# Optimization experiments

Measured on AMD Instinct MI355X. Metric: run time of the kernel, lower is better.

Reference implementation:

```python
import jax, jax.numpy as jnp
import numpy as np

# static sizes (see shape_source)
OBJ_N, WALL_N, FLOOR_N = 192, 16, 1
T = OBJ_N + WALL_N + FLOOR_N          # 209 total nodes
R = T * T - T                          # 43472 directed edges (no self loops)
D = 512
STEPS = 4                              # feat_update_step (1 group)
OBJ_IN, WALL_IN, FLOOR_IN, REL_IN = 42, 15, 16, 2

# buildMap: all-pairs meshgrid edges, self-loops removed, one-hot subj/obj maps
_nd = ~np.eye(T, dtype=bool)
_si, _oi = np.meshgrid(np.arange(T), np.arange(T), indexing='ij')
_subj_idx = _si[_nd]
_obj_idx = _oi[_nd]
SUBJ_MAP = jnp.asarray((np.arange(T)[:, None] == _subj_idx[None, :]).astype(np.float32))  # [T,R]
OBJ_MAP = jnp.asarray((np.arange(T)[:, None] == _obj_idx[None, :]).astype(np.float32))    # [T,R]
TOTAL_MAP = jnp.ones((T, T), jnp.float32)
REL_IDX = jnp.asarray(np.nonzero(_nd.reshape(-1))[0])  # [R] static gather indices


def setup_inputs():
    key = jax.random.key(0)
    ks = iter(jax.random.split(key, 64))
    def w(shape):
        return jax.random.normal(next(ks), shape, jnp.float32) * 0.01  # normal_(0, 0.01)
    inp = {
        'cat_object_feature': jax.random.normal(next(ks), (1, OBJ_N, OBJ_IN), jnp.float32),
        'cat_wall_feature': jax.random.normal(next(ks), (1, WALL_N, WALL_IN), jnp.float32),
        'cat_floor_feature': jax.random.normal(next(ks), (1, FLOOR_N, FLOOR_IN), jnp.float32),
        'cat_relation_feature': jax.random.normal(next(ks), (1, OBJ_N * OBJ_N, REL_IN), jnp.float32),
    }
    for name, din in [('obj', OBJ_IN), ('wall', WALL_IN), ('floor', FLOOR_IN), ('rel', REL_IN)]:
        inp[name + '_w1'] = w((din, D)); inp[name + '_b1'] = jnp.zeros((D,), jnp.float32)
        inp[name + '_w2'] = w((D, D));   inp[name + '_b2'] = jnp.zeros((D,), jnp.float32)
    inp['collect_w'] = w((5, D, D))                       # 5 _Collection_Unit fc weights
    inp['collect_b'] = jnp.zeros((5, D), jnp.float32)
    for name in ['tr', 'eu', 'sc']:
        inp[name + '_w1'] = w((D, D // 2)); inp[name + '_b1'] = jnp.zeros((D // 2,), jnp.float32)
        inp[name + '_w2'] = w((D // 2, 3)); inp[name + '_b2'] = jnp.zeros((3,), jnp.float32)
    return inp


def _mlp(x, w1, b1, w2, b2):
    return jax.nn.relu(x @ w1 + b1) @ w2 + b2


def _head(x, w1, b1, w2, b2):
    # Linear -> LeakyReLU(0.2) -> Dropout(eval: identity) -> Linear
    return jax.nn.leaky_relu(x @ w1 + b1, 0.2) @ w2 + b2


def _collect(src, attn, w, b):
    # _Collection_Unit: attn @ relu(fc(src)) / (row_sum + 1e-7)
    fc = jax.nn.relu(src @ w + b)
    return (attn @ fc) / (attn.sum(1, keepdims=True) + 1e-7)


def reference(cat_object_feature, cat_wall_feature, cat_floor_feature, cat_relation_feature,
              obj_w1, obj_b1, obj_w2, obj_b2, wall_w1, wall_b1, wall_w2, wall_b2,
              floor_w1, floor_b1, floor_w2, floor_b2, rel_w1, rel_b1, rel_w2, rel_b2,
              collect_w, collect_b, tr_w1, tr_b1, tr_w2, tr_b2,
              eu_w1, eu_b1, eu_w2, eu_b2, sc_w1, sc_b1, sc_w2, sc_b2):
    tot = jnp.concatenate([
        _mlp(cat_object_feature[0], obj_w1, obj_b1, obj_w2, obj_b2),
        _mlp(cat_wall_feature[0], wall_w1, wall_b1, wall_w2, wall_b2),
        _mlp(cat_floor_feature[0], floor_w1, floor_b1, floor_w2, floor_b2)], axis=0)  # [T,D]
    emb_rel = _mlp(cat_relation_feature[0], rel_w1, rel_b1, rel_w2, rel_b2)
    padded = jnp.pad(emb_rel.reshape(OBJ_N, OBJ_N, D),
                     ((0, T - OBJ_N), (0, T - OBJ_N), (0, 0)), constant_values=0.001)
    rel = padded.reshape(T * T, D)[REL_IDX]  # mask_total_relation_feature [R,D]

    for _ in range(STEPS):
        s_obj = _collect(tot, TOTAL_MAP, collect_w[4], collect_b[4])
        s_rs = _collect(rel, SUBJ_MAP, collect_w[0], collect_b[0])
        s_ro = _collect(rel, OBJ_MAP, collect_w[1], collect_b[1])
        new_tot = tot + (s_obj + s_rs + s_ro) / 3.0          # _Update_Unit: target + source
        s_os = _collect(tot, SUBJ_MAP.T, collect_w[2], collect_b[2])
        s_oo = _collect(tot, OBJ_MAP.T, collect_w[3], collect_b[3])
        rel = rel + (s_os + s_oo) / 2.0
        tot = new_tot

    obj = tot[:OBJ_N]  # object_mask select
    return jnp.concatenate([
        _head(obj, tr_w1, tr_b1, tr_w2, tr_b2),
        _head(obj, eu_w1, eu_b1, eu_w2, eu_b2),
        _head(obj, sc_w1, sc_b1, sc_w2, sc_b2)], axis=-1)  # [OBJ_N, 9]
```

## Files before the change

kernel.cpp:

```cpp
#include <hip/hip_runtime.h>
#include <stdint.h>

typedef unsigned short u16;
typedef __attribute__((ext_vector_type(4))) float f32x4;
typedef __attribute__((ext_vector_type(8))) short s16x8;
typedef __attribute__((ext_vector_type(4))) short s16x4;

#define DD (512*512)

__device__ inline u16 f2bf(float f) {
  uint32_t u = __float_as_uint(f);
  u = (u + 0x7FFFu + ((u >> 16) & 1u)) >> 16;
  return (u16)u;
}
__device__ inline float bflo(uint32_t w) { return __uint_as_float(w << 16); }
__device__ inline float bfhi(uint32_t w) { return __uint_as_float(w & 0xFFFF0000u); }
__device__ inline f32x4 relu4(f32x4 v) {
  f32x4 r;
  r.x = fmaxf(v.x, 0.f); r.y = fmaxf(v.y, 0.f);
  r.z = fmaxf(v.z, 0.f); r.w = fmaxf(v.w, 0.f);
  return r;
}
__device__ inline f32x4 bf4(const u16* p) {
  uint2 w = *(const uint2*)p;
  f32x4 r; r.x = bflo(w.x); r.y = bfhi(w.x); r.z = bflo(w.y); r.w = bfhi(w.y);
  return r;
}
__device__ inline s16x4 pack4(f32x4 v) {
  s16x4 o;
  o[0] = (short)f2bf(v.x); o[1] = (short)f2bf(v.y);
  o[2] = (short)f2bf(v.z); o[3] = (short)f2bf(v.w);
  return o;
}
__device__ inline void gload16(const void* g, void* l) {
  __builtin_amdgcn_global_load_lds(
      (const __attribute__((address_space(1))) void*)g,
      (__attribute__((address_space(3))) void*)l, 16, 0, 0);
}

__global__ __launch_bounds__(256) void ktotl1(const float* __restrict__ xo, const float* __restrict__ xw,
                                              const float* __restrict__ xf,
                                              const float* __restrict__ ow1, const float* __restrict__ ob1,
                                              const float* __restrict__ ww1, const float* __restrict__ wb1,
                                              const float* __restrict__ fw1, const float* __restrict__ fb1,
                                              float* __restrict__ hid) {
  int tc = blockIdx.x;
  const float* x; const float* w; const float* b; int K;
  if (tc < 192)      { x = xo + tc * 42;        w = ow1; b = ob1; K = 42; }
  else if (tc < 208) { x = xw + (tc - 192) * 15; w = ww1; b = wb1; K = 15; }
  else               { x = xf;                   w = fw1; b = fb1; K = 16; }
  __shared__ float xs[48];
  int t = threadIdx.x;
  if (t < K) xs[t] = x[t];
  __syncthreads();
  #pragma unroll
  for (int dd = 0; dd < 2; dd++) {
    int d = t + dd * 256;
    float acc = b[d];
    for (int k = 0; k < K; k++) acc = fmaf(xs[k], w[k * 512 + d], acc);
    hid[(size_t)tc * 512 + d] = fmaxf(acc, 0.f);
  }
}

struct SJob { const float* A; const float* B; const float* bias; float* C; u16* Cb; int M; int act; };
struct SJobs { SJob j[8]; int cum[9]; int njobs; };

__global__ __launch_bounds__(256) void ksmall(SJobs js) {
  int bi = blockIdx.x;
  int ji = 0;
  while (ji + 1 < js.njobs && bi >= js.cum[ji + 1]) ji++;
  SJob job = js.j[ji];
  int local = bi - js.cum[ji];
  int mt = local >> 3, nt = local & 7;
  int m0 = mt * 32, n0 = nt * 64;

  __shared__ float As[32 * 36];
  __shared__ float Bs[32 * 64];
  int t = threadIdx.x;
  int row = t >> 3;
  int cg  = (t & 7) * 8;
  f32x4 accA = {0.f,0.f,0.f,0.f}, accB = {0.f,0.f,0.f,0.f};

  for (int k0 = 0; k0 < 512; k0 += 32) {
    __syncthreads();
    {
      int ar = t >> 3, ac = (t & 7) * 4;
      f32x4 av = {0.f,0.f,0.f,0.f};
      if (m0 + ar < job.M) av = *(const f32x4*)&job.A[(size_t)(m0 + ar) * 512 + k0 + ac];
      *(f32x4*)&As[ar * 36 + ac] = av;
    }
    #pragma unroll
    for (int i = 0; i < 2; i++) {
      int idx = t + i * 256;
      int bk = idx >> 4, bn = (idx & 15) * 4;
      *(f32x4*)&Bs[bk * 64 + bn] = *(const f32x4*)&job.B[(size_t)(k0 + bk) * 512 + n0 + bn];
    }
    __syncthreads();
    #pragma unroll
    for (int kk = 0; kk < 32; kk += 4) {
      f32x4 a4 = *(const f32x4*)&As[row * 36 + kk];
      #pragma unroll
      for (int q = 0; q < 4; q++) {
        f32x4 b0 = *(const f32x4*)&Bs[(kk + q) * 64 + cg];
        f32x4 b1 = *(const f32x4*)&Bs[(kk + q) * 64 + cg + 4];
        float av = a4[q];
        accA += av * b0;
        accB += av * b1;
      }
    }
  }
  int r = m0 + row;
  if (r < job.M) {
    f32x4 b0 = {0.f,0.f,0.f,0.f}, b1 = {0.f,0.f,0.f,0.f};
    if (job.bias) { b0 = *(const f32x4*)&job.bias[n0 + cg]; b1 = *(const f32x4*)&job.bias[n0 + cg + 4]; }
    f32x4 o0 = accA + b0, o1 = accB + b1;
    if (job.act) { o0 = relu4(o0); o1 = relu4(o1); }
    *(f32x4*)&job.C[(size_t)r * 512 + n0 + cg]     = o0;
    *(f32x4*)&job.C[(size_t)r * 512 + n0 + cg + 4] = o1;
    if (job.Cb) {
      s16x8 ob;
      ob[0] = (short)f2bf(o0.x); ob[1] = (short)f2bf(o0.y);
      ob[2] = (short)f2bf(o0.z); ob[3] = (short)f2bf(o0.w);
      ob[4] = (short)f2bf(o1.x); ob[5] = (short)f2bf(o1.y);
      ob[6] = (short)f2bf(o1.z); ob[7] = (short)f2bf(o1.w);
      *(s16x8*)&job.Cb[(size_t)r * 512 + n0 + cg] = ob;
    }
  }
}

__global__ __launch_bounds__(256) void kcast(const float* __restrict__ src, u16* __restrict__ dst) {
  int g = blockIdx.x * 256 + threadIdx.x;
  f32x4 a = *(const f32x4*)&src[(size_t)g * 8];
  f32x4 b = *(const f32x4*)&src[(size_t)g * 8 + 4];
  s16x8 o;
  o[0] = (short)f2bf(a.x); o[1] = (short)f2bf(a.y); o[2] = (short)f2bf(a.z); o[3] = (short)f2bf(a.w);
  o[4] = (short)f2bf(b.x); o[5] = (short)f2bf(b.y); o[6] = (short)f2bf(b.z); o[7] = (short)f2bf(b.w);
  *(s16x8*)&dst[(size_t)g * 8] = o;
}

__global__ __launch_bounds__(256) void kwcast(const float* __restrict__ cw, u16* __restrict__ cwT) {
  __shared__ float tile[32][33];
  const float* src = cw + (size_t)blockIdx.z * DD;
  int k0 = blockIdx.x * 32, n0 = blockIdx.y * 32;
  int t = threadIdx.x;
  #pragma unroll
  for (int i = 0; i < 4; i++) {
    int idx = t + i * 256; int r = idx >> 5, c = idx & 31;
    tile[r][c] = src[(size_t)(k0 + r) * 512 + n0 + c];
  }
  __syncthreads();
  #pragma unroll
  for (int i = 0; i < 4; i++) {
    int idx = t + i * 256; int r = idx >> 5, c = idx & 31;
    cwT[((size_t)blockIdx.z * 512 + n0 + r) * 512 + k0 + c] = f2bf(tile[c][r]);
  }
}

__global__ __launch_bounds__(256) void kwct(const float* __restrict__ tmp0, const float* __restrict__ tmp1,
                                            u16* __restrict__ WcT) {
  __shared__ float tile[32][33];
  const float* src = blockIdx.z ? tmp1 : tmp0;
  int k0 = blockIdx.x * 32, n0 = blockIdx.y * 32;
  int t = threadIdx.x;
  #pragma unroll
  for (int i = 0; i < 4; i++) {
    int idx = t + i * 256; int r = idx >> 5, c = idx & 31;
    tile[r][c] = src[(size_t)(k0 + r) * 512 + n0 + c];
  }
  __syncthreads();
  #pragma unroll
  for (int i = 0; i < 4; i++) {
    int idx = t + i * 256; int r = idx >> 5, c = idx & 31;
    WcT[((size_t)blockIdx.z * 512 + n0 + r) * 512 + k0 + c] = f2bf(tile[c][r]);
  }
}

__global__ __launch_bounds__(256) void kmisc(const float* __restrict__ cw, const float* __restrict__ cb,
                                             const float* __restrict__ rb2,
                                             float* __restrict__ b0b, float* __restrict__ b0p,
                                             float* __restrict__ b1b, float* __restrict__ b1p) {
  int t = threadIdx.x;
  int dl = t & 63;
  int d = blockIdx.x * 64 + dl;
  int kg = t >> 6;
  const float* W0 = cw;
  const float* W1 = cw + DD;
  float a0 = 0, p0 = 0, a1 = 0, p1 = 0;
  for (int k = kg * 128; k < (kg + 1) * 128; ++k) {
    float w0 = W0[(size_t)k * 512 + d], w1 = W1[(size_t)k * 512 + d], r = rb2[k];
    a0 = fmaf(r, w0, a0); p0 += w0;
    a1 = fmaf(r, w1, a1); p1 += w1;
  }
  __shared__ float red[4][4][64];
  red[0][kg][dl] = a0; red[1][kg][dl] = p0; red[2][kg][dl] = a1; red[3][kg][dl] = p1;
  __syncthreads();
  if (kg == 0) {
    float s0  = red[0][0][dl] + red[0][1][dl] + red[0][2][dl] + red[0][3][dl];
    float sp0 = red[1][0][dl] + red[1][1][dl] + red[1][2][dl] + red[1][3][dl];
    float s1  = red[2][0][dl] + red[2][1][dl] + red[2][2][dl] + red[2][3][dl];
    float sp1 = red[3][0][dl] + red[3][1][dl] + red[3][2][dl] + red[3][3][dl];
    float bb0 = cb[0 * 512 + d], bb1 = cb[1 * 512 + d];
    b0b[d] = s0 + bb0;
    b0p[d] = 0.001f * sp0 + bb0;
    b1b[d] = s1 + bb1;
    b1p[d] = 0.001f * sp1 + bb1;
  }
}

__global__ __launch_bounds__(256) void kH(const float* __restrict__ xr, const float* __restrict__ rw1,
                                          const float* __restrict__ rb1, u16* __restrict__ Hh) {
  int gid = blockIdx.x * 256 + threadIdx.x;
  int m = gid >> 6;
  int dg = (gid & 63) * 8;
  float x0 = xr[m * 2], x1 = xr[m * 2 + 1];
  s16x8 o;
  #pragma unroll
  for (int j = 0; j < 8; j++) {
    int dd = dg + j;
    float v = fmaf(x0, rw1[dd], fmaf(x1, rw1[512 + dd], rb1[dd]));
    o[j] = (short)f2bf(fmaxf(v, 0.f));
  }
  *(s16x8*)&Hh[(size_t)m * 512 + dg] = o;
}

struct MJob { const u16* A; const u16* BT; const float* bias; float* C; int Mreal; int act; };
struct MJobs { MJob j[8]; int cum[9]; int njobs; };

__global__ __launch_bounds__(256) void kmg(MJobs js) {
  int bi = blockIdx.x;
  int ji = 0;
  while (ji + 1 < js.njobs && bi >= js.cum[ji + 1]) ji++;
  MJob job = js.j[ji];
  int local = bi - js.cum[ji];
  int m0 = (local >> 2) * 64, n0 = (local & 3) * 128;

  __shared__ u16 smem[2 * 12288];
  const int t = threadIdx.x;
  const int lane = t & 63;
  const int wave = t >> 6;
  const int wm = wave >> 1, wn = wave & 1;
  const int r16 = lane & 15;
  const int kq = lane >> 4;
  f32x4 acc[2][4];
  #pragma unroll
  for (int i = 0; i < 2; i++)
    #pragma unroll
    for (int j = 0; j < 4; j++) acc[i][j] = (f32x4){0.f,0.f,0.f,0.f};

  const u16* gA[2]; int laofs[2];
  const u16* gB[4]; int lbofs[4];
  #pragma unroll
  for (int i = 0; i < 2; i++) {
    int seg = i * 256 + t;
    int row = seg >> 3, s = seg & 7;
    gA[i] = job.A + (size_t)(m0 + row) * 512 + ((s ^ (row & 7)) << 3);
    laofs[i] = (i * 256 + (t & 192)) << 3;
  }
  #pragma unroll
  for (int i = 0; i < 4; i++) {
    int seg = i * 256 + t;
    int row = seg >> 3, s = seg & 7;
    gB[i] = job.BT + (size_t)(n0 + row) * 512 + ((s ^ (row & 7)) << 3);
    lbofs[i] = 4096 + ((i * 256 + (t & 192)) << 3);
  }

  #pragma unroll
  for (int i = 0; i < 2; i++) gload16(gA[i], smem + laofs[i]);
  #pragma unroll
  for (int i = 0; i < 4; i++) gload16(gB[i], smem + lbofs[i]);
  __syncthreads();

  int buf = 0;
  for (int it = 0; it < 8; ++it) {
    if (it < 7) {
      int nb = (buf ^ 1) * 12288;
      int k0n = (it + 1) * 64;
      #pragma unroll
      for (int i = 0; i < 2; i++) gload16(gA[i] + k0n, smem + nb + laofs[i]);
      #pragma unroll
      for (int i = 0; i < 4; i++) gload16(gB[i] + k0n, smem + nb + lbofs[i]);
    }
    const u16* Ab = smem + buf * 12288;
    const u16* Bb = Ab + 4096;
    #pragma unroll
    for (int kh = 0; kh < 2; kh++) {
      s16x8 af[2], bfr[4];
      #pragma unroll
      for (int i = 0; i < 2; i++) {
        int r = wm * 32 + i * 16 + r16;
        af[i] = *(const s16x8*)&Ab[r * 64 + (((kq + kh * 4) ^ (r & 7)) << 3)];
      }
      #pragma unroll
      for (int j = 0; j < 4; j++) {
        int r = wn * 64 + j * 16 + r16;
        bfr[j] = *(const s16x8*)&Bb[r * 64 + (((kq + kh * 4) ^ (r & 7)) << 3)];
      }
      #pragma unroll
      for (int i = 0; i < 2; i++)
        #pragma unroll
        for (int j = 0; j < 4; j++)
          acc[i][j] = __builtin_amdgcn_mfma_f32_16x16x32_bf16(af[i], bfr[j], acc[i][j], 0, 0, 0);
    }
    __syncthreads();
    buf ^= 1;
  }

  float bj[4] = {0.f, 0.f, 0.f, 0.f};
  if (job.bias) {
    #pragma unroll
    for (int j = 0; j < 4; j++) bj[j] = job.bias[n0 + wn * 64 + j * 16 + r16];
  }
  #pragma unroll
  for (int i = 0; i < 2; i++) {
    int rbase = m0 + wm * 32 + i * 16 + (lane >> 4) * 4;
    #pragma unroll
    for (int r = 0; r < 4; r++) {
      int grow = rbase + r;
      if (grow < job.Mreal) {
        #pragma unroll
        for (int j = 0; j < 4; j++) {
          float v = acc[i][j][r] + bj[j];
          if (job.act) v = fmaxf(v, 0.f);
          job.C[(size_t)grow * 512 + n0 + wn * 64 + j * 16 + r16] = v;
        }
      }
    }
  }
}

__global__ __launch_bounds__(256) void kbig(const u16* __restrict__ Hh, const u16* __restrict__ WcT,
                                            u16* __restrict__ Q0, u16* __restrict__ Q1T) {
  __shared__ u16 smem[2 * 16384];
  const int m0 = blockIdx.y * 128;
  const int n0 = blockIdx.x * 128;
  const int t = threadIdx.x;
  const int lane = t & 63;
  const int wave = t >> 6;
  const int wm = wave >> 1, wn = wave & 1;
  const int r16 = lane & 15;
  const int kq = lane >> 4;
  f32x4 acc[4][4];
  #pragma unroll
  for (int i = 0; i < 4; i++)
    #pragma unroll
    for (int j = 0; j < 4; j++) acc[i][j] = (f32x4){0.f, 0.f, 0.f, 0.f};

  const u16* gA[4]; const u16* gB[4];
  int lofs[4];
  #pragma unroll
  for (int i = 0; i < 4; i++) {
    int seg = i * 256 + t;
    int row = seg >> 3, s = seg & 7;
    int sw = (s ^ (row & 7)) << 3;
    gA[i] = Hh  + (size_t)(m0 + row) * 512 + sw;
    gB[i] = WcT + (size_t)(n0 + row) * 512 + sw;
    lofs[i] = (i * 256 + (t & 192)) << 3;
  }

  #pragma unroll
  for (int i = 0; i < 4; i++) {
    gload16(gA[i], smem + lofs[i]);
    gload16(gB[i], smem + 8192 + lofs[i]);
  }
  __syncthreads();

  int buf = 0;
  for (int it = 0; it < 8; ++it) {
    if (it < 7) {
      int nb = (buf ^ 1) * 16384;
      int k0n = (it + 1) * 64;
      #pragma unroll
      for (int i = 0; i < 4; i++) {
        gload16(gA[i] + k0n, smem + nb + lofs[i]);
        gload16(gB[i] + k0n, smem + nb + 8192 + lofs[i]);
      }
    }
    const u16* Ab = smem + buf * 16384;
    const u16* Bb = Ab + 8192;
    #pragma unroll
    for (int kh = 0; kh < 2; kh++) {
      s16x8 af[4], bfr[4];
      #pragma unroll
      for (int i = 0; i < 4; i++) {
        int r = wm * 64 + i * 16 + r16;
        af[i] = *(const s16x8*)&Ab[r * 64 + (((kq + kh * 4) ^ (r & 7)) << 3)];
      }
      #pragma unroll
      for (int j = 0; j < 4; j++) {
        int r = wn * 64 + j * 16 + r16;
        bfr[j] = *(const s16x8*)&Bb[r * 64 + (((kq + kh * 4) ^ (r & 7)) << 3)];
      }
      #pragma unroll
      for (int i = 0; i < 4; i++)
        #pragma unroll
        for (int j = 0; j < 4; j++)
          acc[i][j] = __builtin_amdgcn_mfma_f32_16x16x32_bf16(af[i], bfr[j], acc[i][j], 0, 0, 0);
    }
    __syncthreads();
    buf ^= 1;
  }

  float* Cs = (float*)smem;
  const bool isQ1 = (n0 >= 512);
  #pragma unroll
  for (int c = 0; c < 4; c++) {
    __syncthreads();
    if ((c >> 1) == wm) {
      const int cbase = (c & 1) * 32;
      #pragma unroll
      for (int ii = 0; ii < 2; ii++) {
        const int i = (cbase >> 4) + ii;
        #pragma unroll
        for (int j = 0; j < 4; j++) {
          #pragma unroll
          for (int r = 0; r < 4; r++) {
            int rrow = i * 16 + (lane >> 4) * 4 + r - cbase;
            int ccol = wn * 64 + j * 16 + r16;
            Cs[rrow * 132 + ccol] = acc[i][j][r];
          }
        }
      }
    }
    __syncthreads();
    const int row = t >> 3, cg = (t & 7) * 16;
    const int gm = m0 + c * 32 + row;
    s16x8 o0, o1;
    #pragma unroll
    for (int x = 0; x < 8; x++) o0[x] = (short)f2bf(Cs[row * 132 + cg + x]);
    #pragma unroll
    for (int x = 0; x < 8; x++) o1[x] = (short)f2bf(Cs[row * 132 + cg + 8 + x]);
    u16* dst;
    if (!isQ1) {
      dst = Q0 + (size_t)gm * 512 + (n0 + cg);
    } else {
      int s = gm / 192, o = gm - s * 192;
      dst = Q1T + ((size_t)o * 192 + s) * 512 + (n0 - 512 + cg);
    }
    *(s16x8*)dst = o0;
    *(s16x8*)(dst + 8) = o1;
  }
}

__global__ __launch_bounds__(128) void kpass(const u16* __restrict__ Q0, const u16* __restrict__ Q1T,
                                             const float* __restrict__ u0, const float* __restrict__ v0,
                                             const float* __restrict__ u1, const float* __restrict__ v1,
                                             const float* __restrict__ b0b, const float* __restrict__ b1b,
                                             const float* __restrict__ fc4,
                                             float* __restrict__ part, float* __restrict__ sobj) {
  int z = blockIdx.z;
  int t = threadIdx.x;
  if (z == 2) {
    if (blockIdx.y != 0 || blockIdx.x >= 4) return;
    int d = blockIdx.x * 128 + t;
    float s = 0.f;
    for (int r = 0; r < 209; ++r) s += fc4[(size_t)r * 512 + d];
    sobj[d] = s;
    return;
  }
  int so = blockIdx.x;
  if (so >= 192) return;
  int chunk = blockIdx.y;
  int d = t * 4;
  const u16* Q = z ? Q1T : Q0;
  const float* fixtab  = z ? v1 : u0;
  const float* looptab = z ? u1 : v0;
  const float* bb = z ? b1b : b0b;
  f32x4 fix = *(const f32x4*)&fixtab[(size_t)so * 512 + d] + *(const f32x4*)&bb[d];
  f32x4 acc = {0.f,0.f,0.f,0.f};
  const u16* qbase = Q + ((size_t)so * 192 + chunk * 48) * 512 + d;
  const float* lbase = looptab + (size_t)(chunk * 48) * 512 + d;
  #pragma unroll 4
  for (int r = 0; r < 48; ++r) {
    f32x4 qa = bf4(qbase + (size_t)r * 512);
    f32x4 vv = *(const f32x4*)(lbase + (size_t)r * 512);
    f32x4 val = qa + fix + vv;
    acc.x += fmaxf(val.x, 0.f); acc.y += fmaxf(val.y, 0.f);
    acc.z += fmaxf(val.z, 0.f); acc.w += fmaxf(val.w, 0.f);
  }
  *(f32x4*)&part[(((size_t)z * 209 + so) * 4 + chunk) * 512 + d] = acc;
}

__global__ __launch_bounds__(128) void kfinish(const u16* __restrict__ Q0, const u16* __restrict__ Q1T,
                                               const float* __restrict__ u0, const float* __restrict__ v0,
                                               const float* __restrict__ u1, const float* __restrict__ v1,
                                               const float* __restrict__ b0b, const float* __restrict__ b0p,
                                               const float* __restrict__ b1b, const float* __restrict__ b1p,
                                               const float* __restrict__ part, const float* __restrict__ sobj,
                                               const float* __restrict__ fcS, const float* __restrict__ fcO,
                                               float* __restrict__ tot, float* __restrict__ addS,
                                               float* __restrict__ addO,
                                               u16* __restrict__ totb, u16* __restrict__ aSb,
                                               u16* __restrict__ aOb) {
  int tt = blockIdx.x;
  int t = threadIdx.x;
  int d = t * 4;
  size_t rowoff = (size_t)tt * 512 + d;
  f32x4 u0r = *(const f32x4*)&u0[rowoff];
  f32x4 v0r = *(const f32x4*)&v0[rowoff];
  f32x4 u1r = *(const f32x4*)&u1[rowoff];
  f32x4 v1r = *(const f32x4*)&v1[rowoff];
  f32x4 B0B = *(const f32x4*)&b0b[d];
  f32x4 B0P = *(const f32x4*)&b0p[d];
  f32x4 B1B = *(const f32x4*)&b1b[d];
  f32x4 B1P = *(const f32x4*)&b1p[d];
  f32x4 srs = {0.f,0.f,0.f,0.f}, sro = {0.f,0.f,0.f,0.f};
  if (tt < 192) {
    #pragma unroll
    for (int c = 0; c < 4; c++) {
      srs += *(const f32x4*)&part[(((size_t)0 * 209 + tt) * 4 + c) * 512 + d];
      sro += *(const f32x4*)&part[(((size_t)1 * 209 + tt) * 4 + c) * 512 + d];
    }
    for (int o = 192; o < 209; o++) srs += relu4(B0P + u0r + *(const f32x4*)&v0[(size_t)o * 512 + d]);
    for (int s = 192; s < 209; s++) sro += relu4(B1P + *(const f32x4*)&u1[(size_t)s * 512 + d] + v1r);
    f32x4 qd0 = bf4(Q0 + ((size_t)tt * 193) * 512 + d);
    srs -= relu4(qd0 + u0r + v0r + B0B);
    f32x4 qd1 = bf4(Q1T + ((size_t)tt * 193) * 512 + d);
    sro -= relu4(qd1 + u1r + v1r + B1B);
  } else {
    for (int o = 0; o < 209; o++) srs += relu4(B0P + u0r + *(const f32x4*)&v0[(size_t)o * 512 + d]);
    srs -= relu4(B0P + u0r + v0r);
    for (int s = 0; s < 209; s++) sro += relu4(B1P + *(const f32x4*)&u1[(size_t)s * 512 + d] + v1r);
    sro -= relu4(B1P + u1r + v1r);
// ... 57 lines not shown
    }
    __syncthreads();
  }
  if (t < 9) {
    const float* B2[3] = {b2a, b2b, b2c};
    out[(size_t)row * 9 + t] = red[t][0] + B2[t / 3][t % 3];
  }
}

extern "C" void kernel_launch(void* const* d_in, const int* in_sizes, int n_in,
                              void* d_out, int out_size, void* d_ws, size_t ws_size,
                              hipStream_t stream) {
  const float* xo  = (const float*)d_in[0];
  const float* xw  = (const float*)d_in[1];
  const float* xf  = (const float*)d_in[2];
  const float* xr  = (const float*)d_in[3];
  const float* ow1 = (const float*)d_in[4];
  const float* ob1 = (const float*)d_in[5];
  const float* ow2 = (const float*)d_in[6];
  const float* ob2 = (const float*)d_in[7];
  const float* ww1 = (const float*)d_in[8];
  const float* wb1 = (const float*)d_in[9];
  const float* ww2 = (const float*)d_in[10];
  const float* wb2 = (const float*)d_in[11];
  const float* fw1 = (const float*)d_in[12];
  const float* fb1 = (const float*)d_in[13];
  const float* fw2 = (const float*)d_in[14];
  const float* fb2 = (const float*)d_in[15];
  const float* rw1 = (const float*)d_in[16];
  const float* rb1 = (const float*)d_in[17];
  const float* rw2 = (const float*)d_in[18];
  const float* rb2 = (const float*)d_in[19];
  const float* cw  = (const float*)d_in[20];
  const float* cb  = (const float*)d_in[21];
  const float* tw1 = (const float*)d_in[22];
  const float* tb1 = (const float*)d_in[23];
  const float* tw2 = (const float*)d_in[24];
  const float* tb2 = (const float*)d_in[25];
  const float* ew1 = (const float*)d_in[26];
  const float* eb1 = (const float*)d_in[27];
  const float* ew2 = (const float*)d_in[28];
  const float* eb2 = (const float*)d_in[29];
  const float* sw1 = (const float*)d_in[30];
  const float* sb1 = (const float*)d_in[31];
  const float* sw2 = (const float*)d_in[32];
  const float* sb2 = (const float*)d_in[33];
  float* out = (float*)d_out;

  char* p = (char*)d_ws;
  auto alloc = [&](size_t bytes) { char* r = p; p += (bytes + 255) & ~(size_t)255; return r; };
  const size_t SZ = 209 * 512 * sizeof(float);
  const size_t BSZ = 256 * 512 * sizeof(u16);
  float* tot  = (float*)alloc(SZ);
  float* addS = (float*)alloc(SZ);
  float* addO = (float*)alloc(SZ);
  u16*   totb = (u16*)alloc(BSZ);
  u16*   aSb  = (u16*)alloc(BSZ);
  u16*   aOb  = (u16*)alloc(BSZ);
  float* fc4  = (float*)alloc(SZ);
  float* fcS  = (float*)alloc(SZ);
  float* fcO  = (float*)alloc(SZ);
  float* u0   = (float*)alloc(SZ);
  float* v0   = (float*)alloc(SZ);
  float* u1   = (float*)alloc(SZ);
  float* v1   = (float*)alloc(SZ);
  float* hid  = (float*)alloc(SZ);
  float* sobj = (float*)alloc(512 * sizeof(float));
  float* part = (float*)alloc((size_t)2 * 209 * 4 * 512 * sizeof(float));
  float* b0b  = (float*)alloc(512 * sizeof(float));
  float* b0p  = (float*)alloc(512 * sizeof(float));
  float* b1b  = (float*)alloc(512 * sizeof(float));
  float* b1p  = (float*)alloc(512 * sizeof(float));
  float* tmp0 = (float*)alloc((size_t)DD * sizeof(float));
  float* tmp1 = (float*)alloc((size_t)DD * sizeof(float));
  u16* rw2b = (u16*)alloc((size_t)DD * sizeof(u16));
  u16* cwT  = (u16*)alloc((size_t)5 * DD * sizeof(u16));
  u16* Hh  = (u16*)alloc((size_t)36864 * 512 * sizeof(u16));
  u16* WcT = (u16*)alloc((size_t)1024 * 512 * sizeof(u16));
  u16* Q0  = (u16*)alloc((size_t)36864 * 512 * sizeof(u16));
  u16* Q1T = (u16*)alloc((size_t)36864 * 512 * sizeof(u16));

  hipMemsetAsync(addS, 0, 2 * SZ + 3 * BSZ, stream);

  ktotl1<<<209, 256, 0, stream>>>(xo, xw, xf, ow1, ob1, ww1, wb1, fw1, fb1, hid);
  kcast<<<128, 256, 0, stream>>>(rw2, rw2b);
  kwcast<<<dim3(16, 16, 5), 256, 0, stream>>>(cw, cwT);

  SJobs pre{};
  pre.j[0] = { hid,             ow2, ob2, tot,             totb,             192, 0 };
  pre.j[1] = { hid + 192 * 512, ww2, wb2, tot + 192 * 512, totb + 192 * 512,  16, 0 };
  pre.j[2] = { hid + 208 * 512, fw2, fb2, tot + 208 * 512, totb + 208 * 512,   1, 0 };
  pre.njobs = 3;
  pre.cum[0] = 0;
  for (int i = 0; i < 3; i++) pre.cum[i + 1] = pre.cum[i] + ((pre.j[i].M + 31) / 32) * 8;
  ksmall<<<pre.cum[3], 256, 0, stream>>>(pre);

  MJobs mpre{};
  mpre.j[0] = { rw2b, cwT,      nullptr, tmp0, 512, 0 };
  mpre.j[1] = { rw2b, cwT + DD, nullptr, tmp1, 512, 0 };
  mpre.njobs = 2;
  mpre.cum[0] = 0; mpre.cum[1] = 32; mpre.cum[2] = 64;
  kmg<<<64, 256, 0, stream>>>(mpre);

  kwct<<<dim3(16, 16, 2), 256, 0, stream>>>(tmp0, tmp1, WcT);
  kmisc<<<8, 256, 0, stream>>>(cw, cb, rb2, b0b, b0p, b1b, b1p);
  kH<<<9216, 256, 0, stream>>>(xr, rw1, rb1, Hh);
  kbig<<<dim3(8, 288), 256, 0, stream>>>(Hh, WcT, Q0, Q1T);

  MJobs st{};
  st.j[0] = { totb, cwT + 4 * DD, cb + 4 * 512, fc4, 209, 1 };
  st.j[1] = { totb, cwT + 2 * DD, cb + 2 * 512, fcS, 209, 1 };
  st.j[2] = { totb, cwT + 3 * DD, cb + 3 * 512, fcO, 209, 1 };
  st.j[3] = { aSb,  cwT,          nullptr,      u0,  209, 0 };
  st.j[4] = { aOb,  cwT,          nullptr,      v0,  209, 0 };
  st.j[5] = { aSb,  cwT + DD,     nullptr,      u1,  209, 0 };
  st.j[6] = { aOb,  cwT + DD,     nullptr,      v1,  209, 0 };
  st.njobs = 7;
  st.cum[0] = 0;
  for (int i = 0; i < 7; i++) st.cum[i + 1] = st.cum[i] + 4 * 4;

  for (int step = 0; step < 4; step++) {
    kmg<<<st.cum[7], 256, 0, stream>>>(st);
    kpass<<<dim3(209, 4, 3), 128, 0, stream>>>(Q0, Q1T, u0, v0, u1, v1, b0b, b1b, fc4, part, sobj);
    kfinish<<<209, 128, 0, stream>>>(Q0, Q1T, u0, v0, u1, v1, b0b, b0p, b1b, b1p,
                                     part, sobj, fcS, fcO, tot, addS, addO, totb, aSb, aOb);
  }

  kheads<<<192, 256, 0, stream>>>(tot, tw1, tb1, tw2, tb2, ew1, eb1, ew2, eb2, sw1, sb1, sw2, sb2, out);
}
```

Before: 458.6 us.

## Merge preprocessing kernels into fused launches and remap kbig blocks per XCD

```diff
diff --git a/kernel.cpp b/kernel.cpp
--- a/kernel.cpp
+++ b/kernel.cpp
@@ -38,121 +38,254 @@
       (__attribute__((address_space(3))) void*)l, 16, 0, 0);
 }
 
-__global__ __launch_bounds__(256) void ktotl1(const float* __restrict__ xo, const float* __restrict__ xw,
-                                              const float* __restrict__ xf,
-                                              const float* __restrict__ ow1, const float* __restrict__ ob1,
-                                              const float* __restrict__ ww1, const float* __restrict__ wb1,
-                                              const float* __restrict__ fw1, const float* __restrict__ fb1,
-                                              float* __restrict__ hid) {
-  int tc = blockIdx.x;
-  const float* x; const float* w; const float* b; int K;
-  if (tc < 192)      { x = xo + tc * 42;        w = ow1; b = ob1; K = 42; }
-  else if (tc < 208) { x = xw + (tc - 192) * 15; w = ww1; b = wb1; K = 15; }
-  else               { x = xf;                   w = fw1; b = fb1; K = 16; }
-  __shared__ float xs[48];
-  int t = threadIdx.x;
-  if (t < K) xs[t] = x[t];
-  __syncthreads();
-  #pragma unroll
-  for (int dd = 0; dd < 2; dd++) {
-    int d = t + dd * 256;
-    float acc = b[d];
-    for (int k = 0; k < K; k++) acc = fmaf(xs[k], w[k * 512 + d], acc);
-    hid[(size_t)tc * 512 + d] = fmaxf(acc, 0.f);
+struct PrepP {
+  const float *xo, *xw, *xf;
+  const float *ow1, *ob1, *ww1, *wb1, *fw1, *fb1;
+  float* hid;
+  const float* rw2; u16* rw2b;
+  const float* cw; u16* cwT;
+  const float* cb; const float* rb2;
+  float *b0b, *b0p, *b1b, *b1p;
+  const float *xr, *rw1, *rb1; u16* Hh;
+};
+
+__global__ __launch_bounds__(256) void kprep(PrepP pp) {
+  __shared__ __align__(16) float plds[1088];
+  const int bid = blockIdx.x;
+  const int t = threadIdx.x;
+  if (bid < 209) {
+    int tc = bid;
+    const float* x; const float* w; const float* b; int K;
+    if (tc < 192)      { x = pp.xo + tc * 42;         w = pp.ow1; b = pp.ob1; K = 42; }
+    else if (tc < 208) { x = pp.xw + (tc - 192) * 15; w = pp.ww1; b = pp.wb1; K = 15; }
+    else               { x = pp.xf;                   w = pp.fw1; b = pp.fb1; K = 16; }
+    float* xs = plds;
+    if (t < K) xs[t] = x[t];
+    __syncthreads();
+    #pragma unroll
+    for (int dd = 0; dd < 2; dd++) {
+      int d = t + dd * 256;
+      float acc = b[d];
+      for (int k = 0; k < K; k++) acc = fmaf(xs[k], w[k * 512 + d], acc);
+      pp.hid[(size_t)tc * 512 + d] = fmaxf(acc, 0.f);
+    }
+  } else if (bid < 337) {
+    int g = (bid - 209) * 256 + t;
+    f32x4 a = *(const f32x4*)&pp.rw2[(size_t)g * 8];
+    f32x4 b = *(const f32x4*)&pp.rw2[(size_t)g * 8 + 4];
+    s16x8 o;
+    o[0] = (short)f2bf(a.x); o[1] = (short)f2bf(a.y); o[2] = (short)f2bf(a.z); o[3] = (short)f2bf(a.w);
+    o[4] = (short)f2bf(b.x); o[5] = (short)f2bf(b.y); o[6] = (short)f2bf(b.z); o[7] = (short)f2bf(b.w);
+    *(s16x8*)&pp.rw2b[(size_t)g * 8] = o;
+  } else if (bid < 1617) {
+    int local = bid - 337;
+    int bx = local & 15, by = (local >> 4) & 15, bz = local >> 8;
+    float (*tile)[33] = (float(*)[33])plds;
+    const float* src = pp.cw + (size_t)bz * DD;
+    int k0 = bx * 32, n0 = by * 32;
+    #pragma unroll
+    for (int i = 0; i < 4; i++) {
+      int idx = t + i * 256; int r = idx >> 5, c = idx & 31;
+      tile[r][c] = src[(size_t)(k0 + r) * 512 + n0 + c];
+    }
+    __syncthreads();
+    #pragma unroll
+    for (int i = 0; i < 4; i++) {
+      int idx = t + i * 256; int r = idx >> 5, c = idx & 31;
+      pp.cwT[((size_t)bz * 512 + n0 + r) * 512 + k0 + c] = f2bf(tile[c][r]);
+    }
+  } else if (bid < 1625) {
+    int bx = bid - 1617;
+    int dl = t & 63;
+    int d = bx * 64 + dl;
+    int kg = t >> 6;
+    const float* W0 = pp.cw;
+    const float* W1 = pp.cw + DD;
+    float a0 = 0, p0 = 0, a1 = 0, p1 = 0;
+    for (int k = kg * 128; k < (kg + 1) * 128; ++k) {
+      float w0 = W0[(size_t)k * 512 + d], w1 = W1[(size_t)k * 512 + d], r = pp.rb2[k];
+      a0 = fmaf(r, w0, a0); p0 += w0;
+      a1 = fmaf(r, w1, a1); p1 += w1;
+    }
+    float (*red)[4][64] = (float(*)[4][64])plds;
+    red[0][kg][dl] = a0; red[1][kg][dl] = p0; red[2][kg][dl] = a1; red[3][kg][dl] = p1;
+    __syncthreads();
+    if (kg == 0) {
+      float s0  = red[0][0][dl] + red[0][1][dl] + red[0][2][dl] + red[0][3][dl];
+      float sp0 = red[1][0][dl] + red[1][1][dl] + red[1][2][dl] + red[1][3][dl];
+      float s1  = red[2][0][dl] + red[2][1][dl] + red[2][2][dl] + red[2][3][dl];
+      float sp1 = red[3][0][dl] + red[3][1][dl] + red[3][2][dl] + red[3][3][dl];
+      float bb0 = pp.cb[0 * 512 + d], bb1 = pp.cb[1 * 512 + d];
+      pp.b0b[d] = s0 + bb0;
+      pp.b0p[d] = 0.001f * sp0 + bb0;
+      pp.b1b[d] = s1 + bb1;
+      pp.b1p[d] = 0.001f * sp1 + bb1;
+    }
+  } else {
+    int gid = (bid - 1625) * 256 + t;
+    int m = gid >> 6;
+    int dg = (gid & 63) * 8;
+    float x0 = pp.xr[m * 2], x1 = pp.xr[m * 2 + 1];
+    s16x8 o;
+    #pragma unroll
+    for (int j = 0; j < 8; j++) {
+      int dd = dg + j;
+      float v = fmaf(x0, pp.rw1[dd], fmaf(x1, pp.rw1[512 + dd], pp.rb1[dd]));
+      o[j] = (short)f2bf(fmaxf(v, 0.f));
+    }
+    *(s16x8*)&pp.Hh[(size_t)m * 512 + dg] = o;
   }
 }
 
 struct SJob { const float* A; const float* B; const float* bias; float* C; u16* Cb; int M; int act; };
-struct SJobs { SJob j[8]; int cum[9]; int njobs; };
-
-__global__ __launch_bounds__(256) void ksmall(SJobs js) {
-  int bi = blockIdx.x;
-  int ji = 0;
-  while (ji + 1 < js.njobs && bi >= js.cum[ji + 1]) ji++;
-  SJob job = js.j[ji];
-  int local = bi - js.cum[ji];
-  int mt = local >> 3, nt = local & 7;
-  int m0 = mt * 32, n0 = nt * 64;
-
-  __shared__ float As[32 * 36];
-  __shared__ float Bs[32 * 64];
-  int t = threadIdx.x;
-  int row = t >> 3;
-  int cg  = (t & 7) * 8;
-  f32x4 accA = {0.f,0.f,0.f,0.f}, accB = {0.f,0.f,0.f,0.f};
-
-  for (int k0 = 0; k0 < 512; k0 += 32) {
-    __syncthreads();
-    {
-      int ar = t >> 3, ac = (t & 7) * 4;
-      f32x4 av = {0.f,0.f,0.f,0.f};
-      if (m0 + ar < job.M) av = *(const f32x4*)&job.A[(size_t)(m0 + ar) * 512 + k0 + ac];
-      *(f32x4*)&As[ar * 36 + ac] = av;
-    }
+struct SJobs { SJob j[4]; int cum[5]; int njobs; };
+struct PMJob { const u16* A; const u16* BT; float* C; };
+struct MidP { SJobs sj; PMJob mj[2]; };
+
+__global__ __launch_bounds__(256) void kmid(MidP mp) {
+  __shared__ __align__(16) u16 mlds[24576];
+  const int t = threadIdx.x;
+  if (blockIdx.x < 64) {
+    int bi = blockIdx.x;
+    int ji = 0;
+    while (ji + 1 < mp.sj.njobs && bi >= mp.sj.cum[ji + 1]) ji++;
+    SJob job = mp.sj.j[ji];
+    int local = bi - mp.sj.cum[ji];
+    int mt = local >> 3, nt = local & 7;
+    int m0 = mt * 32, n0 = nt * 64;
+    float* As = (float*)mlds;
+    float* Bs = As + 32 * 36;
+    int row = t >> 3;
+    int cg  = (t & 7) * 8;
+    f32x4 accA = {0.f,0.f,0.f,0.f}, accB = {0.f,0.f,0.f,0.f};
+    for (int k0 = 0; k0 < 512; k0 += 32) {
+      __syncthreads();
+      {
+        int ar = t >> 3, ac = (t & 7) * 4;
+        f32x4 av = {0.f,0.f,0.f,0.f};
+        if (m0 + ar < job.M) av = *(const f32x4*)&job.A[(size_t)(m0 + ar) * 512 + k0 + ac];
+        *(f32x4*)&As[ar * 36 + ac] = av;
+      }
+      #pragma unroll
+      for (int i = 0; i < 2; i++) {
+        int idx = t + i * 256;
+        int bk = idx >> 4, bn = (idx & 15) * 4;
+        *(f32x4*)&Bs[bk * 64 + bn] = *(const f32x4*)&job.B[(size_t)(k0 + bk) * 512 + n0 + bn];
+      }
+      __syncthreads();
+      #pragma unroll
+      for (int kk = 0; kk < 32; kk += 4) {
+        f32x4 a4 = *(const f32x4*)&As[row * 36 + kk];
+        #pragma unroll
+        for (int q = 0; q < 4; q++) {
+          f32x4 b0 = *(const f32x4*)&Bs[(kk + q) * 64 + cg];
+          f32x4 b1 = *(const f32x4*)&Bs[(kk + q) * 64 + cg + 4];
+          float av = a4[q];
+          accA += av * b0;
+          accB += av * b1;
+        }
+      }
+    }
+    int r = m0 + row;
+    if (r < job.M) {
+      f32x4 b0 = {0.f,0.f,0.f,0.f}, b1 = {0.f,0.f,0.f,0.f};
+      if (job.bias) { b0 = *(const f32x4*)&job.bias[n0 + cg]; b1 = *(const f32x4*)&job.bias[n0 + cg + 4]; }
+      f32x4 o0 = accA + b0, o1 = accB + b1;
+      if (job.act) { o0 = relu4(o0); o1 = relu4(o1); }
+      *(f32x4*)&job.C[(size_t)r * 512 + n0 + cg]     = o0;
+      *(f32x4*)&job.C[(size_t)r * 512 + n0 + cg + 4] = o1;
+      if (job.Cb) {
+        s16x8 ob;
+        ob[0] = (short)f2bf(o0.x); ob[1] = (short)f2bf(o0.y);
+        ob[2] = (short)f2bf(o0.z); ob[3] = (short)f2bf(o0.w);
+        ob[4] = (short)f2bf(o1.x); ob[5] = (short)f2bf(o1.y);
+        ob[6] = (short)f2bf(o1.z); ob[7] = (short)f2bf(o1.w);
+        *(s16x8*)&job.Cb[(size_t)r * 512 + n0 + cg] = ob;
+      }
+    }
+  } else {
+    int bi = blockIdx.x - 64;
+    int ji = bi >> 5;
+    int local = bi & 31;
+    PMJob job = mp.mj[ji];
+    int m0 = (local >> 2) * 64, n0 = (local & 3) * 128;
+    u16* smem = mlds;
+    const int lane = t & 63;
+    const int wave = t >> 6;
+    const int wm = wave >> 1, wn = wave & 1;
+    const int r16 = lane & 15;
+    const int kq = lane >> 4;
+    f32x4 acc[2][4];
+    #pragma unroll
+    for (int i = 0; i < 2; i++)
+      #pragma unroll
+      for (int j = 0; j < 4; j++) acc[i][j] = (f32x4){0.f,0.f,0.f,0.f};
+    const u16* gA[2]; int laofs[2];
+    const u16* gB[4]; int lbofs[4];
     #pragma unroll
     for (int i = 0; i < 2; i++) {
-      int idx = t + i * 256;
-      int bk = idx >> 4, bn = (idx & 15) * 4;
-      *(f32x4*)&Bs[bk * 64 + bn] = *(const f32x4*)&job.B[(size_t)(k0 + bk) * 512 + n0 + bn];
-    }
-    __syncthreads();
-    #pragma unroll
-    for (int kk = 0; kk < 32; kk += 4) {
-      f32x4 a4 = *(const f32x4*)&As[row * 36 + kk];
-      #pragma unroll
-      for (int q = 0; q < 4; q++) {
-        f32x4 b0 = *(const f32x4*)&Bs[(kk + q) * 64 + cg];
-        f32x4 b1 = *(const f32x4*)&Bs[(kk + q) * 64 + cg + 4];
-        float av = a4[q];
-        accA += av * b0;
-        accB += av * b1;
-      }
-    }
-  }
-  int r = m0 + row;
-  if (r < job.M) {
-    f32x4 b0 = {0.f,0.f,0.f,0.f}, b1 = {0.f,0.f,0.f,0.f};
-    if (job.bias) { b0 = *(const f32x4*)&job.bias[n0 + cg]; b1 = *(const f32x4*)&job.bias[n0 + cg + 4]; }
-    f32x4 o0 = accA + b0, o1 = accB + b1;
-    if (job.act) { o0 = relu4(o0); o1 = relu4(o1); }
-    *(f32x4*)&job.C[(size_t)r * 512 + n0 + cg]     = o0;
-    *(f32x4*)&job.C[(size_t)r * 512 + n0 + cg + 4] = o1;
-    if (job.Cb) {
-      s16x8 ob;
-      ob[0] = (short)f2bf(o0.x); ob[1] = (short)f2bf(o0.y);
-      ob[2] = (short)f2bf(o0.z); ob[3] = (short)f2bf(o0.w);
-      ob[4] = (short)f2bf(o1.x); ob[5] = (short)f2bf(o1.y);
-      ob[6] = (short)f2bf(o1.z); ob[7] = (short)f2bf(o1.w);
-      *(s16x8*)&job.Cb[(size_t)r * 512 + n0 + cg] = ob;
-    }
-  }
-}
-
-__global__ __launch_bounds__(256) void kcast(const float* __restrict__ src, u16* __restrict__ dst) {
-  int g = blockIdx.x * 256 + threadIdx.x;
-  f32x4 a = *(const f32x4*)&src[(size_t)g * 8];
-  f32x4 b = *(const f32x4*)&src[(size_t)g * 8 + 4];
-  s16x8 o;
-  o[0] = (short)f2bf(a.x); o[1] = (short)f2bf(a.y); o[2] = (short)f2bf(a.z); o[3] = (short)f2bf(a.w);
-  o[4] = (short)f2bf(b.x); o[5] = (short)f2bf(b.y); o[6] = (short)f2bf(b.z); o[7] = (short)f2bf(b.w);
-  *(s16x8*)&dst[(size_t)g * 8] = o;
-}
-
-__global__ __launch_bounds__(256) void kwcast(const float* __restrict__ cw, u16* __restrict__ cwT) {
-  __shared__ float tile[32][33];
-  const float* src = cw + (size_t)blockIdx.z * DD;
-  int k0 = blockIdx.x * 32, n0 = blockIdx.y * 32;
-  int t = threadIdx.x;
-  #pragma unroll
-  for (int i = 0; i < 4; i++) {
-    int idx = t + i * 256; int r = idx >> 5, c = idx & 31;
-    tile[r][c] = src[(size_t)(k0 + r) * 512 + n0 + c];
-  }
-  __syncthreads();
-  #pragma unroll
-  for (int i = 0; i < 4; i++) {
-    int idx = t + i * 256; int r = idx >> 5, c = idx & 31;
-    cwT[((size_t)blockIdx.z * 512 + n0 + r) * 512 + k0 + c] = f2bf(tile[c][r]);
+      int seg = i * 256 + t;
+      int row = seg >> 3, s = seg & 7;
+      gA[i] = job.A + (size_t)(m0 + row) * 512 + ((s ^ (row & 7)) << 3);
+      laofs[i] = (i * 256 + (t & 192)) << 3;
+    }
+    #pragma unroll
+    for (int i = 0; i < 4; i++) {
+      int seg = i * 256 + t;
+      int row = seg >> 3, s = seg & 7;
+      gB[i] = job.BT + (size_t)(n0 + row) * 512 + ((s ^ (row & 7)) << 3);
+      lbofs[i] = 4096 + ((i * 256 + (t & 192)) << 3);
+    }
+    #pragma unroll
+    for (int i = 0; i < 2; i++) gload16(gA[i], smem + laofs[i]);
+    #pragma unroll
+    for (int i = 0; i < 4; i++) gload16(gB[i], smem + lbofs[i]);
+    __syncthreads();
+    int buf = 0;
+    for (int it = 0; it < 8; ++it) {
+      if (it < 7) {
+        int nb = (buf ^ 1) * 12288;
+        int k0n = (it + 1) * 64;
+        #pragma unroll
+        for (int i = 0; i < 2; i++) gload16(gA[i] + k0n, smem + nb + laofs[i]);
+        #pragma unroll
+        for (int i = 0; i < 4; i++) gload16(gB[i] + k0n, smem + nb + lbofs[i]);
+      }
+      const u16* Ab = smem + buf * 12288;
+      const u16* Bb = Ab + 4096;
+      #pragma unroll
+      for (int kh = 0; kh < 2; kh++) {
+        s16x8 af[2], bfr[4];
+        #pragma unroll
+        for (int i = 0; i < 2; i++) {
+          int r = wm * 32 + i * 16 + r16;
+          af[i] = *(const s16x8*)&Ab[r * 64 + (((kq + kh * 4) ^ (r & 7)) << 3)];
+        }
+        #pragma unroll
+        for (int j = 0; j < 4; j++) {
+          int r = wn * 64 + j * 16 + r16;
+          bfr[j] = *(const s16x8*)&Bb[r * 64 + (((kq + kh * 4) ^ (r & 7)) << 3)];
+        }
+        #pragma unroll
+        for (int i = 0; i < 2; i++)
+          #pragma unroll
+          for (int j = 0; j < 4; j++)
+            acc[i][j] = __builtin_amdgcn_mfma_f32_16x16x32_bf16(af[i], bfr[j], acc[i][j], 0, 0, 0);
+      }
+      __syncthreads();
+      buf ^= 1;
+    }
+    #pragma unroll
+    for (int i = 0; i < 2; i++) {
+      int rbase = m0 + wm * 32 + i * 16 + (lane >> 4) * 4;
+      #pragma unroll
+      for (int r = 0; r < 4; r++) {
+        int grow = rbase + r;
+        #pragma unroll
+        for (int j = 0; j < 4; j++)
+          job.C[(size_t)grow * 512 + n0 + wn * 64 + j * 16 + r16] = acc[i][j][r];
+      }
+    }
   }
 }
 
@@ -175,52 +308,118 @@
   }
 }
 
-__global__ __launch_bounds__(256) void kmisc(const float* __restrict__ cw, const float* __restrict__ cb,
-                                             const float* __restrict__ rb2,
-                                             float* __restrict__ b0b, float* __restrict__ b0p,
-                                             float* __restrict__ b1b, float* __restrict__ b1p) {
-  int t = threadIdx.x;
-  int dl = t & 63;
-  int d = blockIdx.x * 64 + dl;
-  int kg = t >> 6;
-  const float* W0 = cw;
-  const float* W1 = cw + DD;
-  float a0 = 0, p0 = 0, a1 = 0, p1 = 0;
-  for (int k = kg * 128; k < (kg + 1) * 128; ++k) {
-    float w0 = W0[(size_t)k * 512 + d], w1 = W1[(size_t)k * 512 + d], r = rb2[k];
-    a0 = fmaf(r, w0, a0); p0 += w0;
-    a1 = fmaf(r, w1, a1); p1 += w1;
-  }
-  __shared__ float red[4][4][64];
-  red[0][kg][dl] = a0; red[1][kg][dl] = p0; red[2][kg][dl] = a1; red[3][kg][dl] = p1;
+__global__ __launch_bounds__(256) void kbig(const u16* __restrict__ Hh, const u16* __restrict__ WcT,
+                                            u16* __restrict__ Q0, u16* __restrict__ Q1T) {
+  __shared__ u16 smem[2 * 16384];
+  const int bid = blockIdx.x;
+  const int xcd = bid & 7;
+  const int lp = bid >> 3;
+  const int m0 = (xcd * 36 + (lp >> 3)) * 128;
+  const int n0 = (lp & 7) * 128;
+  const int t = threadIdx.x;
+  const int lane = t & 63;
+  const int wave = t >> 6;
+  const int wm = wave >> 1, wn = wave & 1;
+  const int r16 = lane & 15;
+  const int kq = lane >> 4;
+  f32x4 acc[4][4];
+  #pragma unroll
+  for (int i = 0; i < 4; i++)
+    #pragma unroll
+    for (int j = 0; j < 4; j++) acc[i][j] = (f32x4){0.f, 0.f, 0.f, 0.f};
+
+  const u16* gA[4]; const u16* gB[4];
+  int lofs[4];
+  #pragma unroll
+  for (int i = 0; i < 4; i++) {
+    int seg = i * 256 + t;
+    int row = seg >> 3, s = seg & 7;
+    int sw = (s ^ (row & 7)) << 3;
+    gA[i] = Hh  + (size_t)(m0 + row) * 512 + sw;
+    gB[i] = WcT + (size_t)(n0 + row) * 512 + sw;
+    lofs[i] = (i * 256 + (t & 192)) << 3;
+  }
+  #pragma unroll
+  for (int i = 0; i < 4; i++) {
+    gload16(gA[i], smem + lofs[i]);
+    gload16(gB[i], smem + 8192 + lofs[i]);
+  }
   __syncthreads();
-  if (kg == 0) {
-    float s0  = red[0][0][dl] + red[0][1][dl] + red[0][2][dl] + red[0][3][dl];
-    float sp0 = red[1][0][dl] + red[1][1][dl] + red[1][2][dl] + red[1][3][dl];
-    float s1  = red[2][0][dl] + red[2][1][dl] + red[2][2][dl] + red[2][3][dl];
-    float sp1 = red[3][0][dl] + red[3][1][dl] + red[3][2][dl] + red[3][3][dl];
-    float bb0 = cb[0 * 512 + d], bb1 = cb[1 * 512 + d];
-    b0b[d] = s0 + bb0;
-    b0p[d] = 0.001f * sp0 + bb0;
-    b1b[d] = s1 + bb1;
-    b1p[d] = 0.001f * sp1 + bb1;
-  }
-}
-
-__global__ __launch_bounds__(256) void kH(const float* __restrict__ xr, const float* __restrict__ rw1,
-                                          const float* __restrict__ rb1, u16* __restrict__ Hh) {
-  int gid = blockIdx.x * 256 + threadIdx.x;
-  int m = gid >> 6;
-  int dg = (gid & 63) * 8;
-  float x0 = xr[m * 2], x1 = xr[m * 2 + 1];
-  s16x8 o;
-  #pragma unroll
-  for (int j = 0; j < 8; j++) {
-    int dd = dg + j;
-    float v = fmaf(x0, rw1[dd], fmaf(x1, rw1[512 + dd], rb1[dd]));
-    o[j] = (short)f2bf(fmaxf(v, 0.f));
-  }
-  *(s16x8*)&Hh[(size_t)m * 512 + dg] = o;
+  int buf = 0;
+  for (int it = 0; it < 8; ++it) {
+    if (it < 7) {
+      int nb = (buf ^ 1) * 16384;
+      int k0n = (it + 1) * 64;
+      #pragma unroll
+      for (int i = 0; i < 4; i++) {
+        gload16(gA[i] + k0n, smem + nb + lofs[i]);
+        gload16(gB[i] + k0n, smem + nb + 8192 + lofs[i]);
+      }
+    }
+    const u16* Ab = smem + buf * 16384;
+    const u16* Bb = Ab + 8192;
+    #pragma unroll
+    for (int kh = 0; kh < 2; kh++) {
+      s16x8 af[4], bfr[4];
+      #pragma unroll
+      for (int i = 0; i < 4; i++) {
+        int r = wm * 64 + i * 16 + r16;
+        af[i] = *(const s16x8*)&Ab[r * 64 + (((kq + kh * 4) ^ (r & 7)) << 3)];
+      }
+      #pragma unroll
+      for (int j = 0; j < 4; j++) {
+        int r = wn * 64 + j * 16 + r16;
+        bfr[j] = *(const s16x8*)&Bb[r * 64 + (((kq + kh * 4) ^ (r & 7)) << 3)];
+      }
+      #pragma unroll
+      for (int i = 0; i < 4; i++)
+        #pragma unroll
+        for (int j = 0; j < 4; j++)
+          acc[i][j] = __builtin_amdgcn_mfma_f32_16x16x32_bf16(af[i], bfr[j], acc[i][j], 0, 0, 0);
+    }
+    __syncthreads();
+    buf ^= 1;
+  }
+
+  float* Cs = (float*)smem;
+  const bool isQ1 = (n0 >= 512);
+  #pragma unroll
+  for (int c = 0; c < 4; c++) {
+    __syncthreads();
+    if ((c >> 1) == wm) {
+      const int cbase = (c & 1) * 32;
+      #pragma unroll
+      for (int ii = 0; ii < 2; ii++) {
+        const int i = (cbase >> 4) + ii;
+        #pragma unroll
+        for (int j = 0; j < 4; j++) {
+          #pragma unroll
+          for (int r = 0; r < 4; r++) {
+            int rrow = i * 16 + (lane >> 4) * 4 + r - cbase;
+            int ccol = wn * 64 + j * 16 + r16;
+            Cs[rrow * 132 + ccol] = acc[i][j][r];
+          }
+        }
+      }
+    }
+    __syncthreads();
+    const int row = t >> 3, cg = (t & 7) * 16;
+    const int gm = m0 + c * 32 + row;
+    s16x8 o0, o1;
+    #pragma unroll
+    for (int x = 0; x < 8; x++) o0[x] = (short)f2bf(Cs[row * 132 + cg + x]);
+    #pragma unroll
+    for (int x = 0; x < 8; x++) o1[x] = (short)f2bf(Cs[row * 132 + cg + 8 + x]);
+    u16* dst;
+    if (!isQ1) {
+      dst = Q0 + (size_t)gm * 512 + (n0 + cg);
+    } else {
+      int s = gm / 192, o = gm - s * 192;
+      dst = Q1T + ((size_t)o * 192 + s) * 512 + (n0 - 512 + cg);
+    }
+    *(s16x8*)dst = o0;
+    *(s16x8*)(dst + 8) = o1;
+  }
 }
 
 struct MJob { const u16* A; const u16* BT; const float* bias; float* C; int Mreal; int act; };
@@ -325,119 +524,6 @@
         }
       }
     }
-  }
-}
-
-__global__ __launch_bounds__(256) void kbig(const u16* __restrict__ Hh, const u16* __restrict__ WcT,
-                                            u16* __restrict__ Q0, u16* __restrict__ Q1T) {
-  __shared__ u16 smem[2 * 16384];
-  const int m0 = blockIdx.y * 128;
-  const int n0 = blockIdx.x * 128;
-  const int t = threadIdx.x;
-  const int lane = t & 63;
-  const int wave = t >> 6;
-  const int wm = wave >> 1, wn = wave & 1;
-  const int r16 = lane & 15;
-  const int kq = lane >> 4;
-  f32x4 acc[4][4];
-  #pragma unroll
-  for (int i = 0; i < 4; i++)
-    #pragma unroll
-    for (int j = 0; j < 4; j++) acc[i][j] = (f32x4){0.f, 0.f, 0.f, 0.f};
-
-  const u16* gA[4]; const u16* gB[4];
-  int lofs[4];
-  #pragma unroll
-  for (int i = 0; i < 4; i++) {
-    int seg = i * 256 + t;
-    int row = seg >> 3, s = seg & 7;
-    int sw = (s ^ (row & 7)) << 3;
-    gA[i] = Hh  + (size_t)(m0 + row) * 512 + sw;
-    gB[i] = WcT + (size_t)(n0 + row) * 512 + sw;
-    lofs[i] = (i * 256 + (t & 192)) << 3;
-  }
-
-  #pragma unroll
-  for (int i = 0; i < 4; i++) {
-    gload16(gA[i], smem + lofs[i]);
-    gload16(gB[i], smem + 8192 + lofs[i]);
-  }
-  __syncthreads();
-
-  int buf = 0;
-  for (int it = 0; it < 8; ++it) {
-    if (it < 7) {
-      int nb = (buf ^ 1) * 16384;
-      int k0n = (it + 1) * 64;
-      #pragma unroll
-      for (int i = 0; i < 4; i++) {
-        gload16(gA[i] + k0n, smem + nb + lofs[i]);
-        gload16(gB[i] + k0n, smem + nb + 8192 + lofs[i]);
-      }
-    }
-    const u16* Ab = smem + buf * 16384;
-    const u16* Bb = Ab + 8192;
-    #pragma unroll
-    for (int kh = 0; kh < 2; kh++) {
-      s16x8 af[4], bfr[4];
-      #pragma unroll
-      for (int i = 0; i < 4; i++) {
-        int r = wm * 64 + i * 16 + r16;
-        af[i] = *(const s16x8*)&Ab[r * 64 + (((kq + kh * 4) ^ (r & 7)) << 3)];
-      }
-      #pragma unroll
-      for (int j = 0; j < 4; j++) {
-        int r = wn * 64 + j * 16 + r16;
-        bfr[j] = *(const s16x8*)&Bb[r * 64 + (((kq + kh * 4) ^ (r & 7)) << 3)];
-      }
-      #pragma unroll
-      for (int i = 0; i < 4; i++)
-        #pragma unroll
-        for (int j = 0; j < 4; j++)
-          acc[i][j] = __builtin_amdgcn_mfma_f32_16x16x32_bf16(af[i], bfr[j], acc[i][j], 0, 0, 0);
-    }
-    __syncthreads();
-    buf ^= 1;
-  }
-
-  float* Cs = (float*)smem;
-  const bool isQ1 = (n0 >= 512);
-  #pragma unroll
-  for (int c = 0; c < 4; c++) {
-    __syncthreads();
-    if ((c >> 1) == wm) {
-      const int cbase = (c & 1) * 32;
-      #pragma unroll
-      for (int ii = 0; ii < 2; ii++) {
-        const int i = (cbase >> 4) + ii;
-        #pragma unroll
-        for (int j = 0; j < 4; j++) {
-          #pragma unroll
-          for (int r = 0; r < 4; r++) {
-            int rrow = i * 16 + (lane >> 4) * 4 + r - cbase;
-            int ccol = wn * 64 + j * 16 + r16;
-            Cs[rrow * 132 + ccol] = acc[i][j][r];
-          }
-        }
-      }
-    }
-    __syncthreads();
-    const int row = t >> 3, cg = (t & 7) * 16;
-    const int gm = m0 + c * 32 + row;
-    s16x8 o0, o1;
-    #pragma unroll
-    for (int x = 0; x < 8; x++) o0[x] = (short)f2bf(Cs[row * 132 + cg + x]);
-    #pragma unroll
-    for (int x = 0; x < 8; x++) o1[x] = (short)f2bf(Cs[row * 132 + cg + 8 + x]);
-    u16* dst;
-    if (!isQ1) {
-      dst = Q0 + (size_t)gm * 512 + (n0 + cg);
-    } else {
-      int s = gm / 192, o = gm - s * 192;
-      dst = Q1T + ((size_t)o * 192 + s) * 512 + (n0 - 512 + cg);
-    }
-    *(s16x8*)dst = o0;
-    *(s16x8*)(dst + 8) = o1;
   }
 }
 
@@ -661,30 +747,30 @@
 
   hipMemsetAsync(addS, 0, 2 * SZ + 3 * BSZ, stream);
 
-  ktotl1<<<209, 256, 0, stream>>>(xo, xw, xf, ow1, ob1, ww1, wb1, fw1, fb1, hid);
-  kcast<<<128, 256, 0, stream>>>(rw2, rw2b);
-  kwcast<<<dim3(16, 16, 5), 256, 0, stream>>>(cw, cwT);
-
-  SJobs pre{};
-  pre.j[0] = { hid,             ow2, ob2, tot,             totb,             192, 0 };
-  pre.j[1] = { hid + 192 * 512, ww2, wb2, tot + 192 * 512, totb + 192 * 512,  16, 0 };
-  pre.j[2] = { hid + 208 * 512, fw2, fb2, tot + 208 * 512, totb + 208 * 512,   1, 0 };
-  pre.njobs = 3;
-  pre.cum[0] = 0;
-  for (int i = 0; i < 3; i++) pre.cum[i + 1] = pre.cum[i] + ((pre.j[i].M + 31) / 32) * 8;
-  ksmall<<<pre.cum[3], 256, 0, stream>>>(pre);
-
-  MJobs mpre{};
-  mpre.j[0] = { rw2b, cwT,      nullptr, tmp0, 512, 0 };
-  mpre.j[1] = { rw2b, cwT + DD, nullptr, tmp1, 512, 0 };
-  mpre.njobs = 2;
-  mpre.cum[0] = 0; mpre.cum[1] = 32; mpre.cum[2] = 64;
-  kmg<<<64, 256, 0, stream>>>(mpre);
+  PrepP pp;
+  pp.xo = xo; pp.xw = xw; pp.xf = xf;
+  pp.ow1 = ow1; pp.ob1 = ob1; pp.ww1 = ww1; pp.wb1 = wb1; pp.fw1 = fw1; pp.fb1 = fb1;
+  pp.hid = hid;
+  pp.rw2 = rw2; pp.rw2b = rw2b;
+  pp.cw = cw; pp.cwT = cwT;
+  pp.cb = cb; pp.rb2 = rb2;
+  pp.b0b = b0b; pp.b0p = b0p; pp.b1b = b1b; pp.b1p = b1p;
+  pp.xr = xr; pp.rw1 = rw1; pp.rb1 = rb1; pp.Hh = Hh;
+  kprep<<<10841, 256, 0, stream>>>(pp);
+
+  MidP mp{};
+  mp.sj.j[0] = { hid,             ow2, ob2, tot,             totb,             192, 0 };
+  mp.sj.j[1] = { hid + 192 * 512, ww2, wb2, tot + 192 * 512, totb + 192 * 512,  16, 0 };
+  mp.sj.j[2] = { hid + 208 * 512, fw2, fb2, tot + 208 * 512, totb + 208 * 512,   1, 0 };
+  mp.sj.njobs = 3;
+  mp.sj.cum[0] = 0;
+  for (int i = 0; i < 3; i++) mp.sj.cum[i + 1] = mp.sj.cum[i] + ((mp.sj.j[i].M + 31) / 32) * 8;
+  mp.mj[0] = { rw2b, cwT,      tmp0 };
+  mp.mj[1] = { rw2b, cwT + DD, tmp1 };
+  kmid<<<128, 256, 0, stream>>>(mp);
 
   kwct<<<dim3(16, 16, 2), 256, 0, stream>>>(tmp0, tmp1, WcT);
-  kmisc<<<8, 256, 0, stream>>>(cw, cb, rb2, b0b, b0p, b1b, b1p);
-  kH<<<9216, 256, 0, stream>>>(xr, rw1, rb1, Hh);
-  kbig<<<dim3(8, 288), 256, 0, stream>>>(Hh, WcT, Q0, Q1T);
+  kbig<<<2304, 256, 0, stream>>>(Hh, WcT, Q0, Q1T);
 
   MJobs st{};
   st.j[0] = { totb, cwT + 4 * DD, cb + 4 * 512, fc4, 209, 1 };
```

Measured after the change: 414.0 us. -9.7%, faster.
